# Kernel tuning notes

Hardware: AMD Instinct MI355X
Metric: run time of the kernel (lower is better)

## Reference

```python
import jax, jax.numpy as jnp
import numpy as np

N, D, K = 32768, 256, 2048
BETA = 0.25  # init arg beta, in [0,1) branch of the loss


def setup_inputs() -> dict:
    key = jax.random.key(0)
    k1, k2 = jax.random.split(key)
    x = jax.random.normal(k1, (N, D), dtype=jnp.float32)
    # mimics nn.Embedding init: uniform(-1/K, 1/K) then mean-centered
    cb = jax.random.uniform(k2, (K, D), dtype=jnp.float32, minval=-1.0 / K, maxval=1.0 / K)
    codebook = cb - cb.mean(axis=0)
    return {"x": x, "codebook": codebook}


def reference(x, codebook):
    # pairwise squared L2 distances: [N, K]
    dist = (
        jnp.sum(x * x, axis=1, keepdims=True)
        + jnp.sum(codebook * codebook, axis=1)
        - 2.0 * jnp.matmul(x, codebook.T)
    )
    encoding_inds = jnp.argmin(dist, axis=1)  # [N]
    # one-hot @ codebook == gather of nearest code vectors
    x_codebook = jnp.take(codebook, encoding_inds, axis=0)  # [N, D]
    # straight-through quantization
    x_quantized = x + jax.lax.stop_gradient(x_codebook - x)
    # VQ loss, beta in [0, 1) branch
    commit = jnp.mean((x - jax.lax.stop_gradient(x_codebook)) ** 2)
    embed = jnp.mean((x_codebook - jax.lax.stop_gradient(x)) ** 2)
    loss = BETA * commit + embed
    return x_quantized, loss
```

## Files before the change

### kernel.cpp

```cpp
#include <hip/hip_runtime.h>

#define N_ROWS 32768
#define DIM    256
#define KCODES 2048
#define CSCALE 4096.0f

typedef __attribute__((ext_vector_type(16))) float f32x16;
typedef __attribute__((ext_vector_type(4)))  unsigned int u32x4;

union frag16 { u32x4 v; long l[2]; };

#define SWAIT(s) asm volatile("s_waitcnt " s)

__device__ __forceinline__ void gl16(const void* g, void* l) {
    __builtin_amdgcn_global_load_lds(
        (const __attribute__((address_space(1))) unsigned int*)g,
        (__attribute__((address_space(3))) unsigned int*)l, 16, 0, 0);
}

__device__ __forceinline__ u32x4 ldsr128(const void* p) {
    const unsigned a =
        (unsigned)(unsigned long long)(__attribute__((address_space(3))) const char*)p;
    u32x4 d;
    asm volatile("ds_read_b128 %0, %1" : "=&v"(d) : "v"(a));
    return d;
}

__device__ __forceinline__ uint4 pack16(const float* s) {
    int a = __builtin_amdgcn_cvt_pk_fp8_f32(s[0],  s[1],  0, false);
    a     = __builtin_amdgcn_cvt_pk_fp8_f32(s[2],  s[3],  a, true);
    int b = __builtin_amdgcn_cvt_pk_fp8_f32(s[4],  s[5],  0, false);
    b     = __builtin_amdgcn_cvt_pk_fp8_f32(s[6],  s[7],  b, true);
    int c = __builtin_amdgcn_cvt_pk_fp8_f32(s[8],  s[9],  0, false);
    c     = __builtin_amdgcn_cvt_pk_fp8_f32(s[10], s[11], c, true);
    int d = __builtin_amdgcn_cvt_pk_fp8_f32(s[12], s[13], 0, false);
    d     = __builtin_amdgcn_cvt_pk_fp8_f32(s[14], s[15], d, true);
    uint4 o; o.x = a; o.y = b; o.z = c; o.w = d;
    return o;
}


__global__ void prep_cb(const float* __restrict__ cb, unsigned int* __restrict__ cbf8,
                        float* __restrict__ halfcn, float* __restrict__ loss) {
    const int t    = threadIdx.x;
    const int code = blockIdx.x * 4 + (t >> 6);
    const int s    = t & 63;
    if (blockIdx.x == 0 && t == 0) *loss = 0.0f;
    const int kc = s >> 4, d = (s >> 2) & 3, b4 = (s & 3) * 4;
    const int h = d >> 1, q = d & 1;
    const int k0 = kc * 64 + q * 32 + (b4 >> 3) * 16 + h * 8 + (b4 & 7);
    float4 v = *(const float4*)&cb[(size_t)code * DIM + k0];
    int pk = __builtin_amdgcn_cvt_pk_fp8_f32(v.x * CSCALE, v.y * CSCALE, 0, false);
    pk     = __builtin_amdgcn_cvt_pk_fp8_f32(v.z * CSCALE, v.w * CSCALE, pk, true);
    cbf8[(size_t)code * 64 + s] = (unsigned int)pk;
    float ssum = v.x * v.x + v.y * v.y + v.z * v.z + v.w * v.w;
    #pragma unroll
    for (int o = 32; o > 0; o >>= 1) ssum += __shfl_down(ssum, o, 64);
    if (s == 0) halfcn[code] = 0.5f * CSCALE * ssum;
}

__global__ __launch_bounds__(256, 2) void vq_fused(
        const float* __restrict__ x, const float* __restrict__ cb,
        const char* __restrict__ cbf8, const float* __restrict__ halfcn,
        float* __restrict__ out, float* __restrict__ loss) {
    __shared__ char As[4][4096];
    __shared__ char Bs[3][4][4096];
    __shared__ float hcs[KCODES];
    __shared__ float red[64][4];
    __shared__ int  idxs[64];
    __shared__ float lred[4];

    const int t    = threadIdx.x;
    const int lane = t & 63;
    const int w    = t >> 6;
    const int l32  = lane & 31;
    const int h    = lane >> 5;
    const int row0 = blockIdx.x * 64;

    {
        const int r   = t >> 2;
        const int kc  = t & 3;
        const int key = (r >> 1) & 3;
        const float* src = x + (size_t)(row0 + r) * DIM + kc * 64;
        float buf[16];
        #pragma unroll
        for (int p = 0; p < 4; p++) {
            const int d = p ^ key, hh = d >> 1, qq = d & 1;
            #pragma unroll
            for (int j = 0; j < 4; j++) *(float4*)(buf + j * 4) =
                *(const float4*)(src + qq * 32 + (j >> 1) * 16 + hh * 8 + (j & 1) * 4);
            *(uint4*)(As[kc] + r * 64 + p * 16) = pack16(buf);
        }
        #pragma unroll
        for (int j = 0; j < 8; j++) hcs[j * 256 + t] = halfcn[j * 256 + t];
    }

    const int lsub = lane >> 2;
    const int lpos = lane & 3;
    auto stageB = [&](int j) {
        const int pass_ = j >> 2, kc_ = j & 3;
        char* dst = Bs[j % 3][w];
        #pragma unroll
        for (int r_ = 0; r_ < 4; r_++) {
            const int lc = r_ * 16 + lsub;
            const int g  = lpos ^ ((lc >> 1) & 3);
            const char* src = cbf8 + (size_t)(pass_ * 256 + w * 64 + lc) * 256
                              + kc_ * 64 + g * 16;
            gl16(src, dst + r_ * 1024);
        }
    };

    const int key = (l32 >> 1) & 3;
    const int p0  = (h * 2 + 0) ^ key;
    const int p1  = (h * 2 + 1) ^ key;

    frag16 afr[4][2][2];
    frag16 bf[2][2][2];

    float mp[2][16];
    #pragma unroll
    for (int rt = 0; rt < 2; rt++)
        #pragma unroll
        for (int r = 0; r < 16; r++) mp[rt][r] = -3.0e38f;

    __syncthreads();

    #pragma unroll
    for (int kc = 0; kc < 4; kc++) {
        const char* ab = As[kc];
        #pragma unroll
        for (int rt = 0; rt < 2; rt++) {
            const int rbase = (rt * 32 + l32) * 64;
            afr[kc][rt][0].v = *(const u32x4*)(ab + rbase + p0 * 16);
            afr[kc][rt][1].v = *(const u32x4*)(ab + rbase + p1 * 16);
        }
    }

    stageB(0); stageB(1); stageB(2);
    SWAIT("vmcnt(8)");
    {
        const char* bb = Bs[0][w];
        #pragma unroll
        for (int ct = 0; ct < 2; ct++) {
            const int cbase = (ct * 32 + l32) * 64;
            bf[0][ct][0].v = ldsr128(bb + cbase + p0 * 16);
            bf[0][ct][1].v = ldsr128(bb + cbase + p1 * 16);
        }
    }

    #pragma unroll
    for (int pass = 0; pass < 8; ++pass) {
        const float hc0 = hcs[pass * 256 + w * 64 + l32];
        const float hc1 = hcs[pass * 256 + w * 64 + 32 + l32];
        f32x16 acc[2][2];
        #pragma unroll
        for (int rt = 0; rt < 2; rt++)
            #pragma unroll
            for (int r = 0; r < 16; r++) {
                acc[rt][0][r] = -hc0;
                acc[rt][1][r] = -hc1;
            }

        #pragma unroll
        for (int kc = 0; kc < 4; ++kc) {
            const int i  = pass * 4 + kc;
            const int cs = kc & 1;
            const int ns = cs ^ 1;

            SWAIT("lgkmcnt(0)");
            __builtin_amdgcn_sched_barrier(0);

            if (i + 3 < 32) {
                stageB(i + 3);
                SWAIT("vmcnt(8)");
            } else if (i == 29) {
                SWAIT("vmcnt(4)");
            } else if (i == 30) {
                SWAIT("vmcnt(0)");
            }

            if (i + 1 < 32) {
                const char* bb = Bs[(i + 1) % 3][w];
                #pragma unroll
                for (int ct = 0; ct < 2; ct++) {
                    const int cbase = (ct * 32 + l32) * 64;
                    bf[ns][ct][0].v = ldsr128(bb + cbase + p0 * 16);
                    bf[ns][ct][1].v = ldsr128(bb + cbase + p1 * 16);
                }
            }

            __builtin_amdgcn_s_setprio(1);
            #pragma unroll
            for (int q = 0; q < 2; q++)
                #pragma unroll
                for (int hf = 0; hf < 2; hf++)
                    #pragma unroll
                    for (int rt = 0; rt < 2; rt++)
                        #pragma unroll
                        for (int ct = 0; ct < 2; ct++)
                            acc[rt][ct] = __builtin_amdgcn_mfma_f32_32x32x16_fp8_fp8(
                                afr[kc][rt][q].l[hf], bf[cs][ct][q].l[hf],
                                acc[rt][ct], 0, 0, 0);
            __builtin_amdgcn_s_setprio(0);
        }

        #pragma unroll
        for (int ct = 0; ct < 2; ct++) {
            const unsigned code = (unsigned)(pass * 256 + w * 64 + ct * 32 + l32);
            #pragma unroll
            for (int rt = 0; rt < 2; rt++)
                #pragma unroll
                for (int r = 0; r < 16; r++) {
                    unsigned u = (__float_as_uint(acc[rt][ct][r]) & 0xFFFFF800u) | code;
                    mp[rt][r] = fmaxf(mp[rt][r], __uint_as_float(u));
                }
        }
    }

    #pragma unroll
    for (int m = 1; m <= 16; m <<= 1)
        #pragma unroll
        for (int rt = 0; rt < 2; rt++)
            #pragma unroll
            for (int r = 0; r < 16; r++)
                mp[rt][r] = fmaxf(mp[rt][r], __shfl_xor(mp[rt][r], m, 64));

    if (l32 == 0) {
        #pragma unroll
        for (int rt = 0; rt < 2; rt++)
            #pragma unroll
            for (int r = 0; r < 16; r++) {
                const int row = rt * 32 + (r & 3) + 8 * (r >> 2) + 4 * h;
                red[row][w] = mp[rt][r];
            }
    }
    __syncthreads();
    if (t < 64) {
        float b0 = fmaxf(fmaxf(red[t][0], red[t][1]), fmaxf(red[t][2], red[t][3]));
        idxs[t] = (int)(__float_as_uint(b0) & 2047u);
    }
    __syncthreads();

    float lsum = 0.0f;
    #pragma unroll 4
    for (int r = 0; r < 64; r++) {
        const int code = idxs[r];
        const float c  = cb[(size_t)code * DIM + t];
        const float xv = x[(size_t)(row0 + r) * DIM + t];
        out[(size_t)(row0 + r) * DIM + t] = c;
        const float d = xv - c;
        lsum += d * d;
    }
    #pragma unroll
    for (int o = 32; o > 0; o >>= 1) lsum += __shfl_down(lsum, o, 64);
    if (lane == 0) lred[w] = lsum;
    __syncthreads();
    if (t == 0) {
        const float scale = 1.25f / (float)((size_t)N_ROWS * DIM);
        atomicAdd(loss, (lred[0] + lred[1] + lred[2] + lred[3]) * scale);
    }
}

extern "C" void kernel_launch(void* const* d_in, const int* in_sizes, int n_in,
                              void* d_out, int out_size, void* d_ws, size_t ws_size,
                              hipStream_t stream) {
    const float* x  = (const float*)d_in[0];
    const float* cb = (const float*)d_in[1];
    float* out  = (float*)d_out;
    float* loss = out + (size_t)N_ROWS * DIM;

    char* ws = (char*)d_ws;
    unsigned int* cbf8 = (unsigned int*)ws;
    float* halfcn = (float*)(ws + (size_t)KCODES * 256);

    prep_cb<<<KCODES / 4, 256, 0, stream>>>(cb, cbf8, halfcn, loss);
    vq_fused<<<N_ROWS / 64, 256, 0, stream>>>(x, cb, (const char*)cbf8, halfcn, out, loss);
}
```

Baseline: 125.2 us.

## Halve rows per block to raise occupancy and shrink LDS footprint

Each block now handles 32 rows instead of 64. LDS use is cut by moving to a double-buffered codebook stage, keeping the half-norms in registers, and overlaying the reduction scratch on the A tile. The A fragments are streamed from LDS per k-chunk instead of being held for the whole kernel, which lowers register pressure so launch bounds can ask for 4 blocks per CU. In exchange, each block's reuse of the codebook stream is halved, so the fp8 codebook is streamed twice as many times in total, and the shallower prefetch may expose load latency.

```diff
diff --git a/kernel.cpp b/kernel.cpp
--- a/kernel.cpp
+++ b/kernel.cpp
@@ -4,6 +4,7 @@
 #define DIM    256
 #define KCODES 2048
 #define CSCALE 4096.0f
+#define BROWS  32
 
 typedef __attribute__((ext_vector_type(16))) float f32x16;
 typedef __attribute__((ext_vector_type(4)))  unsigned int u32x4;
@@ -59,47 +60,52 @@
     if (s == 0) halfcn[code] = 0.5f * CSCALE * ssum;
 }
 
-__global__ __launch_bounds__(256, 2) void vq_fused(
+__global__ __launch_bounds__(256, 4) void vq_fused(
         const float* __restrict__ x, const float* __restrict__ cb,
         const char* __restrict__ cbf8, const float* __restrict__ halfcn,
         float* __restrict__ out, float* __restrict__ loss) {
-    __shared__ char As[4][4096];
-    __shared__ char Bs[3][4][4096];
-    __shared__ float hcs[KCODES];
-    __shared__ float red[64][4];
-    __shared__ int  idxs[64];
-    __shared__ float lred[4];
+    __shared__ char As[4][2048];
+    __shared__ char Bs[2][4][4096];
+    struct Tail { float red[BROWS][4]; int idxs[BROWS]; float lred[4]; };
+    Tail* tl = (Tail*)As;
 
     const int t    = threadIdx.x;
     const int lane = t & 63;
     const int w    = t >> 6;
     const int l32  = lane & 31;
     const int h    = lane >> 5;
-    const int row0 = blockIdx.x * 64;
+    const int row0 = blockIdx.x * BROWS;
 
     {
-        const int r   = t >> 2;
-        const int kc  = t & 3;
+        const int r   = t >> 3;
+        const int kc  = (t >> 1) & 3;
+        const int pp  = t & 1;
         const int key = (r >> 1) & 3;
         const float* src = x + (size_t)(row0 + r) * DIM + kc * 64;
         float buf[16];
         #pragma unroll
-        for (int p = 0; p < 4; p++) {
+        for (int pi = 0; pi < 2; pi++) {
+            const int p = pp * 2 + pi;
             const int d = p ^ key, hh = d >> 1, qq = d & 1;
             #pragma unroll
             for (int j = 0; j < 4; j++) *(float4*)(buf + j * 4) =
                 *(const float4*)(src + qq * 32 + (j >> 1) * 16 + hh * 8 + (j & 1) * 4);
             *(uint4*)(As[kc] + r * 64 + p * 16) = pack16(buf);
         }
-        #pragma unroll
-        for (int j = 0; j < 8; j++) hcs[j * 256 + t] = halfcn[j * 256 + t];
+    }
+
+    float hcv[8][2];
+    #pragma unroll
+    for (int p = 0; p < 8; p++) {
+        hcv[p][0] = halfcn[p * 256 + w * 64 + l32];
+        hcv[p][1] = halfcn[p * 256 + w * 64 + 32 + l32];
     }
 
     const int lsub = lane >> 2;
     const int lpos = lane & 3;
     auto stageB = [&](int j) {
         const int pass_ = j >> 2, kc_ = j & 3;
-        char* dst = Bs[j % 3][w];
+        char* dst = Bs[j & 1][w];
         #pragma unroll
         for (int r_ = 0; r_ < 4; r_++) {
             const int lc = r_ * 16 + lsub;
@@ -114,30 +120,23 @@
     const int p0  = (h * 2 + 0) ^ key;
     const int p1  = (h * 2 + 1) ^ key;
 
-    frag16 afr[4][2][2];
+    frag16 af[2][2];
     frag16 bf[2][2][2];
 
-    float mp[2][16];
-    #pragma unroll
-    for (int rt = 0; rt < 2; rt++)
-        #pragma unroll
-        for (int r = 0; r < 16; r++) mp[rt][r] = -3.0e38f;
-
-    __syncthreads();
-
-    #pragma unroll
-    for (int kc = 0; kc < 4; kc++) {
-        const char* ab = As[kc];
-        #pragma unroll
-        for (int rt = 0; rt < 2; rt++) {
-            const int rbase = (rt * 32 + l32) * 64;
-            afr[kc][rt][0].v = *(const u32x4*)(ab + rbase + p0 * 16);
-            afr[kc][rt][1].v = *(const u32x4*)(ab + rbase + p1 * 16);
-        }
-    }
-
-    stageB(0); stageB(1); stageB(2);
-    SWAIT("vmcnt(8)");
+    float mp[16];
+    #pragma unroll
+    for (int r = 0; r < 16; r++) mp[r] = -3.0e38f;
+
+    __syncthreads();
+
+    {
+        const char* ab = As[0];
+        const int rbase = l32 * 64;
+        af[0][0].v = ldsr128(ab + rbase + p0 * 16);
+        af[0][1].v = ldsr128(ab + rbase + p1 * 16);
+    }
+    stageB(0); stageB(1);
+    SWAIT("vmcnt(4)");
     {
         const char* bb = Bs[0][w];
         #pragma unroll
@@ -150,16 +149,12 @@
 
     #pragma unroll
     for (int pass = 0; pass < 8; ++pass) {
-        const float hc0 = hcs[pass * 256 + w * 64 + l32];
-        const float hc1 = hcs[pass * 256 + w * 64 + 32 + l32];
-        f32x16 acc[2][2];
-        #pragma unroll
-        for (int rt = 0; rt < 2; rt++)
-            #pragma unroll
-            for (int r = 0; r < 16; r++) {
-                acc[rt][0][r] = -hc0;
-                acc[rt][1][r] = -hc1;
-            }
+        f32x16 acc[2];
+        #pragma unroll
+        for (int r = 0; r < 16; r++) {
+            acc[0][r] = -hcv[pass][0];
+            acc[1][r] = -hcv[pass][1];
+        }
 
         #pragma unroll
         for (int kc = 0; kc < 4; ++kc) {
@@ -170,17 +165,19 @@
             SWAIT("lgkmcnt(0)");
             __builtin_amdgcn_sched_barrier(0);
 
-            if (i + 3 < 32) {
-                stageB(i + 3);
-                SWAIT("vmcnt(8)");
-            } else if (i == 29) {
+            if (i + 2 < 32) {
+                stageB(i + 2);
                 SWAIT("vmcnt(4)");
             } else if (i == 30) {
                 SWAIT("vmcnt(0)");
             }
 
             if (i + 1 < 32) {
-                const char* bb = Bs[(i + 1) % 3][w];
+                const char* ab = As[(kc + 1) & 3];
+                const char* bb = Bs[(i + 1) & 1][w];
+                const int rbase = l32 * 64;
+                af[ns][0].v = ldsr128(ab + rbase + p0 * 16);
+                af[ns][1].v = ldsr128(ab + rbase + p1 * 16);
                 #pragma unroll
                 for (int ct = 0; ct < 2; ct++) {
                     const int cbase = (ct * 32 + l32) * 64;
@@ -195,12 +192,10 @@
                 #pragma unroll
                 for (int hf = 0; hf < 2; hf++)
                     #pragma unroll
-                    for (int rt = 0; rt < 2; rt++)
-                        #pragma unroll
-                        for (int ct = 0; ct < 2; ct++)
-                            acc[rt][ct] = __builtin_amdgcn_mfma_f32_32x32x16_fp8_fp8(
-                                afr[kc][rt][q].l[hf], bf[cs][ct][q].l[hf],
-                                acc[rt][ct], 0, 0, 0);
+                    for (int ct = 0; ct < 2; ct++)
+                        acc[ct] = __builtin_amdgcn_mfma_f32_32x32x16_fp8_fp8(
+                            af[cs][q].l[hf], bf[cs][ct][q].l[hf],
+                            acc[ct], 0, 0, 0);
             __builtin_amdgcn_s_setprio(0);
         }
 
@@ -208,43 +203,40 @@
         for (int ct = 0; ct < 2; ct++) {
             const unsigned code = (unsigned)(pass * 256 + w * 64 + ct * 32 + l32);
             #pragma unroll
-            for (int rt = 0; rt < 2; rt++)
-                #pragma unroll
-                for (int r = 0; r < 16; r++) {
-                    unsigned u = (__float_as_uint(acc[rt][ct][r]) & 0xFFFFF800u) | code;
-                    mp[rt][r] = fmaxf(mp[rt][r], __uint_as_float(u));
-                }
+            for (int r = 0; r < 16; r++) {
+                unsigned u = (__float_as_uint(acc[ct][r]) & 0xFFFFF800u) | code;
+                mp[r] = fmaxf(mp[r], __uint_as_float(u));
+            }
         }
     }
 
     #pragma unroll
     for (int m = 1; m <= 16; m <<= 1)
         #pragma unroll
-        for (int rt = 0; rt < 2; rt++)
-            #pragma unroll
-            for (int r = 0; r < 16; r++)
-                mp[rt][r] = fmaxf(mp[rt][r], __shfl_xor(mp[rt][r], m, 64));
+        for (int r = 0; r < 16; r++)
+            mp[r] = fmaxf(mp[r], __shfl_xor(mp[r], m, 64));
+
+    __syncthreads();
 
     if (l32 == 0) {
         #pragma unroll
-        for (int rt = 0; rt < 2; rt++)
-            #pragma unroll
-            for (int r = 0; r < 16; r++) {
-                const int row = rt * 32 + (r & 3) + 8 * (r >> 2) + 4 * h;
-                red[row][w] = mp[rt][r];
-            }
-    }
-    __syncthreads();
-    if (t < 64) {
-        float b0 = fmaxf(fmaxf(red[t][0], red[t][1]), fmaxf(red[t][2], red[t][3]));
-        idxs[t] = (int)(__float_as_uint(b0) & 2047u);
+        for (int r = 0; r < 16; r++) {
+            const int row = (r & 3) + 8 * (r >> 2) + 4 * h;
+            tl->red[row][w] = mp[r];
+        }
+    }
+    __syncthreads();
+    if (t < BROWS) {
+        float b0 = fmaxf(fmaxf(tl->red[t][0], tl->red[t][1]),
+                         fmaxf(tl->red[t][2], tl->red[t][3]));
+        tl->idxs[t] = (int)(__float_as_uint(b0) & 2047u);
     }
     __syncthreads();
 
     float lsum = 0.0f;
     #pragma unroll 4
-    for (int r = 0; r < 64; r++) {
-        const int code = idxs[r];
+    for (int r = 0; r < BROWS; r++) {
+        const int code = tl->idxs[r];
         const float c  = cb[(size_t)code * DIM + t];
         const float xv = x[(size_t)(row0 + r) * DIM + t];
         out[(size_t)(row0 + r) * DIM + t] = c;
@@ -253,11 +245,11 @@
     }
     #pragma unroll
     for (int o = 32; o > 0; o >>= 1) lsum += __shfl_down(lsum, o, 64);
-    if (lane == 0) lred[w] = lsum;
+    if (lane == 0) tl->lred[w] = lsum;
     __syncthreads();
     if (t == 0) {
         const float scale = 1.25f / (float)((size_t)N_ROWS * DIM);
-        atomicAdd(loss, (lred[0] + lred[1] + lred[2] + lred[3]) * scale);
+        atomicAdd(loss, (tl->lred[0] + tl->lred[1] + tl->lred[2] + tl->lred[3]) * scale);
     }
 }
 
@@ -274,5 +266,5 @@
     float* halfcn = (float*)(ws + (size_t)KCODES * 256);
 
     prep_cb<<<KCODES / 4, 256, 0, stream>>>(cb, cbf8, halfcn, loss);
-    vq_fused<<<N_ROWS / 64, 256, 0, stream>>>(x, cb, (const char*)cbf8, halfcn, out, loss);
-}
+    vq_fused<<<N_ROWS / BROWS, 256, 0, stream>>>(x, cb, (const char*)cbf8, halfcn, out, loss);
+}
```

Result: slower. 151.1 us (+20.6%).
